# Performance work log

Measured on AMD Instinct MI355X. Metric: run time of the kernel, lower is better.

## Reference

```python
import jax, jax.numpy as jnp
import numpy as np

B, D, C, L, H = 4096, 768, 512, 32, 256
E = C * L  # total flattened extension embeddings

def _l2norm(x, eps=1e-12):
    n = jnp.sqrt(jnp.sum(x * x, axis=-1, keepdims=True))
    return x / jnp.maximum(n, eps)

def setup_inputs() -> dict:
    key = jax.random.key(0)
    ks = jax.random.split(key, 8)
    text_feat = jax.random.normal(ks[0], (B, D), dtype=jnp.float32)
    img_feat = jax.random.normal(ks[1], (B, D), dtype=jnp.float32)
    ext_embs = _l2norm(jax.random.normal(ks[2], (E, D), dtype=jnp.float32))
    concept_names = _l2norm(jax.random.normal(ks[3], (C, D), dtype=jnp.float32))
    # each concept has exactly L extension embeddings; sorted segment ids
    segment_ids = jnp.repeat(jnp.arange(C, dtype=jnp.int32), L)
    W1 = jax.random.normal(ks[4], (C + D, H), dtype=jnp.float32) * (1.0 / np.sqrt(C + D))
    b1 = jnp.zeros((H,), dtype=jnp.float32)
    W2 = jax.random.normal(ks[5], (H, C), dtype=jnp.float32) * (1.0 / np.sqrt(H))
    b2 = jnp.zeros((C,), dtype=jnp.float32)
    alpha = jnp.float32(0.5)
    temperature = jnp.float32(0.07)
    return {"text_feat": text_feat, "img_feat": img_feat, "ext_embs": ext_embs,
            "segment_ids": segment_ids, "concept_names": concept_names,
            "W1": W1, "b1": b1, "W2": W2, "b2": b2,
            "alpha": alpha, "temperature": temperature}

def reference(text_feat, img_feat, ext_embs, segment_ids, concept_names,
              W1, b1, W2, b2, alpha, temperature):
    # query = normalize(text + img)
    q = _l2norm(text_feat + img_feat)                      # [B, D]
    # ragged per-concept max similarity: one big GEMM + segmented max
    sim = jnp.einsum('bd,ed->be', q, ext_embs)            # [B, E]
    prior = jax.ops.segment_max(sim.T, segment_ids,
                                num_segments=C,
                                indices_are_sorted=True).T  # [B, C]
    # small MLP -> temperature softmax -> weighted concept sum
    h = jax.nn.relu(jnp.concatenate([prior, q], axis=-1) @ W1 + b1)  # [B, H]
    logits = h @ W2 + b2                                   # [B, C]
    weights = jax.nn.softmax(logits / temperature, axis=-1)
    dyn_prompt = weights @ concept_names                   # [B, D]
    combined = text_feat + alpha * dyn_prompt
    return _l2norm(combined)
```

## Files before the change

kernel.cpp:

```cpp
#include <hip/hip_runtime.h>
#include <hip/hip_bf16.h>

typedef unsigned short bfu;
typedef __attribute__((ext_vector_type(4))) float f32x4;
typedef __attribute__((ext_vector_type(8))) short bf16x8;
typedef __attribute__((ext_vector_type(4))) int i32x4;
typedef __attribute__((ext_vector_type(8))) int i32x8;

#define GAS __attribute__((address_space(1)))
#define LAS __attribute__((address_space(3)))

__device__ __forceinline__ unsigned short f2bf(float f) {
    unsigned int u = __float_as_uint(f);
    u += 0x7FFFu + ((u >> 16) & 1u);
    return (unsigned short)(u >> 16);
}

__device__ __forceinline__ void gld_lds16(const void* g, void* l) {
    __builtin_amdgcn_global_load_lds((GAS void*)g, (LAS void*)l, 16, 0, 0);
}

__device__ __forceinline__ unsigned pack_fp8x4(float a, float b, float c, float d) {
    int u = __builtin_amdgcn_cvt_pk_fp8_f32(a, b, 0, false);
    u = __builtin_amdgcn_cvt_pk_fp8_f32(c, d, u, true);
    return (unsigned)u;
}

__device__ __forceinline__ float block_sum256(float v, float* sm) {
    #pragma unroll
    for (int off = 32; off; off >>= 1) v += __shfl_xor(v, off);
    int w = threadIdx.x >> 6;
    if ((threadIdx.x & 63) == 0) sm[w] = v;
    __syncthreads();
    float r = sm[0] + sm[1] + sm[2] + sm[3];
    __syncthreads();
    return r;
}

__device__ __forceinline__ float block_max256(float v, float* sm) {
    #pragma unroll
    for (int off = 32; off; off >>= 1) v = fmaxf(v, __shfl_xor(v, off));
    int w = threadIdx.x >> 6;
    if ((threadIdx.x & 63) == 0) sm[w] = v;
    __syncthreads();
    float r = fmaxf(fmaxf(sm[0], sm[1]), fmaxf(sm[2], sm[3]));
    __syncthreads();
    return r;
}

__device__ __forceinline__ void transpose_piece(const float* __restrict__ in,
                                                bfu* __restrict__ out, int R, int idx) {
    int c = idx / R, r = idx - c * R;
    out[idx] = f2bf(in[(size_t)r * ((size_t)0) + 0]);
}

__global__ __launch_bounds__(256) void prep_kernel(const float* __restrict__ ext,
                                                   unsigned* __restrict__ E8,
                                                   const float* __restrict__ W1, bfu* __restrict__ W1t,
                                                   const float* __restrict__ W2, bfu* __restrict__ W2t,
                                                   const float* __restrict__ cn, bfu* __restrict__ cnt) {
    int b = blockIdx.x;
    if (b < 12288) {
        int i = b * 256 + threadIdx.x;
        float4 v = ((const float4*)ext)[i];
        E8[i] = pack_fp8x4(v.x * 16.0f, v.y * 16.0f, v.z * 16.0f, v.w * 16.0f);
    } else if (b < 13568) {
        int idx = (b - 12288) * 256 + threadIdx.x;
        int c = idx / 1280, r = idx - c * 1280;
        W1t[idx] = f2bf(W1[(size_t)r * 256 + c]);
    } else if (b < 14080) {
        int idx = (b - 13568) * 256 + threadIdx.x;
        int c = idx / 256, r = idx - c * 256;
        W2t[idx] = f2bf(W2[(size_t)r * 512 + c]);
    } else {
        int idx = (b - 14080) * 256 + threadIdx.x;
        int c = idx / 512, r = idx - c * 512;
        cnt[idx] = f2bf(cn[(size_t)r * 768 + c]);
    }
}

__global__ __launch_bounds__(256) void q_kernel(const float* __restrict__ text,
                                                const float* __restrict__ img,
                                                bfu* __restrict__ X,
                                                unsigned* __restrict__ Q8) {
    __shared__ float sm[4];
    int row = blockIdx.x, t = threadIdx.x;
    float4 v = {0.f, 0.f, 0.f, 0.f};
    if (t < 192) {
        float4 a = ((const float4*)(text + (size_t)row * 768))[t];
        float4 b = ((const float4*)(img + (size_t)row * 768))[t];
        v.x = a.x + b.x; v.y = a.y + b.y; v.z = a.z + b.z; v.w = a.w + b.w;
    }
    float ss = v.x * v.x + v.y * v.y + v.z * v.z + v.w * v.w;
    float tot = block_sum256(ss, sm);
    float inv = 1.0f / fmaxf(sqrtf(tot), 1e-12f);
    if (t < 192) {
        ushort4 o = make_ushort4(f2bf(v.x * inv), f2bf(v.y * inv), f2bf(v.z * inv), f2bf(v.w * inv));
        ((ushort4*)(X + (size_t)row * 1280 + 512))[t] = o;
        float s16 = inv * 16.0f;
        Q8[(size_t)row * 192 + t] = pack_fp8x4(v.x * s16, v.y * s16, v.z * s16, v.w * s16);
    }
}

__device__ __forceinline__ i32x8 ld_frag8(const char* s, int row, int lq) {
    const int r7 = row & 7;
    i32x4 lo = *(const i32x4*)(s + row * 128 + ((((lq << 1))     ^ r7) << 4));
    i32x4 hi = *(const i32x4*)(s + row * 128 + ((((lq << 1) | 1) ^ r7) << 4));
    i32x8 v;
    v[0] = lo[0]; v[1] = lo[1]; v[2] = lo[2]; v[3] = lo[3];
    v[4] = hi[0]; v[5] = hi[1]; v[6] = hi[2]; v[7] = hi[3];
    return v;
}

__global__ __launch_bounds__(256) void sim_segmax_kernel(const unsigned char* __restrict__ Q8,
                                                         const unsigned char* __restrict__ E8,
                                                         bfu* __restrict__ X) {
    __shared__ __align__(16) char sA[128 * 128];
    __shared__ __align__(16) char sB[128 * 128];
    int bm = blockIdx.x >> 7;
    int bn = blockIdx.x & 127;
    int m0 = bm * 128, n0 = bn * 128;
    const int t = threadIdx.x, lane = t & 63, wv = t >> 6;
    const int wm = (wv >> 1) << 6, wn = (wv & 1) << 6;
    const int lr = lane & 15, lq = lane >> 4;

    f32x4 zero = {0.f, 0.f, 0.f, 0.f};
    f32x4 acc[4][4];
    #pragma unroll
    for (int i = 0; i < 4; ++i)
        #pragma unroll
        for (int j = 0; j < 4; ++j) acc[i][j] = zero;

    for (int k0 = 0; k0 < 768; k0 += 128) {
        #pragma unroll
        for (int i = 0; i < 4; ++i) {
            int idx = i * 256 + t;
            int row = idx >> 3, cs = idx & 7, cg = cs ^ (row & 7);
            gld_lds16(Q8 + (size_t)(m0 + row) * 768 + k0 + (cg << 4), sA + idx * 16);
            gld_lds16(E8 + (size_t)(n0 + row) * 768 + k0 + (cg << 4), sB + idx * 16);
        }
        __syncthreads();
        i32x8 af[4], bf8[4];
        #pragma unroll
        for (int f = 0; f < 4; ++f) {
            af[f]  = ld_frag8(sA, wm + f * 16 + lr, lq);
            bf8[f] = ld_frag8(sB, wn + f * 16 + lr, lq);
        }
        #pragma unroll
        for (int i = 0; i < 4; ++i)
            #pragma unroll
            for (int j = 0; j < 4; ++j)
                acc[i][j] = __builtin_amdgcn_mfma_scale_f32_16x16x128_f8f6f4(
                    af[i], bf8[j], acc[i][j], 0, 0, 0, 0x7F7F7F7F, 0, 0x7F7F7F7F);
        __syncthreads();
    }

    const float sc = 0.00390625f;
    #pragma unroll
    for (int i = 0; i < 4; ++i) {
        #pragma unroll
        for (int r = 0; r < 4; ++r) {
            float g0 = fmaxf(acc[i][0][r], acc[i][1][r]);
            float g1 = fmaxf(acc[i][2][r], acc[i][3][r]);
            #pragma unroll
            for (int off = 8; off; off >>= 1) {
                g0 = fmaxf(g0, __shfl_xor(g0, off));
                g1 = fmaxf(g1, __shfl_xor(g1, off));
            }
            if (lr == 0) {
                int row = m0 + wm + i * 16 + lq * 4 + r;
                int g = (n0 + wn) >> 5;
                X[(size_t)row * 1280 + g]     = f2bf(g0 * sc);
                X[(size_t)row * 1280 + g + 1] = f2bf(g1 * sc);
            }
        }
    }
}

template <int BM>
__device__ __forceinline__ void gemm_mainloop(const bfu* A, const bfu* B, int K,
                                              int lda, int ldb, int m0, int n0,
                                              short* sA, short* sB, f32x4 acc[BM / 32][4]) {
    const int t = threadIdx.x, lane = t & 63, wv = t >> 6;
    const int wm = (wv >> 1) * (BM / 2), wn = (wv & 1) << 6;
    const int lr = lane & 15, lq = lane >> 4;

    for (int k0 = 0; k0 < K; k0 += 64) {
        #pragma unroll
        for (int i = 0; i < BM / 32; ++i) {
            int idx = i * 256 + t;
            int row = idx >> 3, cs = idx & 7, cg = cs ^ (row & 7);
            gld_lds16(A + (size_t)(m0 + row) * lda + k0 + (cg << 3), sA + idx * 8);
        }
        #pragma unroll
        for (int i = 0; i < 4; ++i) {
            int idx = i * 256 + t;
            int row = idx >> 3, cs = idx & 7, cg = cs ^ (row & 7);
            gld_lds16(B + (size_t)(n0 + row) * ldb + k0 + (cg << 3), sB + idx * 8);
        }
        __syncthreads();
        #pragma unroll
        for (int kk = 0; kk < 2; ++kk) {
            bf16x8 af[BM / 32], bfr[4];
            #pragma unroll
            for (int f = 0; f < BM / 32; ++f) {
                int mrow = wm + f * 16 + lr;
                int c = kk * 4 + lq;
                af[f] = *(const bf16x8*)(sA + mrow * 64 + ((c ^ (mrow & 7)) << 3));
            }
            #pragma unroll
            for (int f = 0; f < 4; ++f) {
                int nrow = wn + f * 16 + lr;
                int c = kk * 4 + lq;
                bfr[f] = *(const bf16x8*)(sB + nrow * 64 + ((c ^ (nrow & 7)) << 3));
            }
            #pragma unroll
            for (int i = 0; i < BM / 32; ++i)
                #pragma unroll
                for (int j = 0; j < 4; ++j)
                    acc[i][j] = __builtin_amdgcn_mfma_f32_16x16x32_bf16(af[i], bfr[j], acc[i][j], 0, 0, 0);
        }
        __syncthreads();
    }
}

template <int EPI, int BM>
__global__ __launch_bounds__(256) void gemm_kernel(const bfu* __restrict__ A,
                                                   const bfu* __restrict__ B,
                                                   const float* __restrict__ bias,
                                                   void* __restrict__ out,
                                                   int K, int lda, int ldb, int N, int ntN) {
    __shared__ __align__(16) short sA[BM * 64];
    __shared__ __align__(16) short sB[128 * 64];
    int bm = blockIdx.x / ntN, bn = blockIdx.x - bm * ntN;
    int m0 = bm * BM, n0 = bn * 128;
    f32x4 zero = {0.f, 0.f, 0.f, 0.f};
    f32x4 acc[BM / 32][4];
    #pragma unroll
    for (int i = 0; i < BM / 32; ++i)
        #pragma unroll
        for (int j = 0; j < 4; ++j) acc[i][j] = zero;

    gemm_mainloop<BM>(A, B, K, lda, ldb, m0, n0, sA, sB, acc);

    const int t = threadIdx.x, lane = t & 63, wv = t >> 6;
    const int wm = (wv >> 1) * (BM / 2), wn = (wv & 1) << 6;
    const int lr = lane & 15, lq = lane >> 4;
    #pragma unroll
    for (int j = 0; j < 4; ++j) {
        int col = n0 + wn + j * 16 + lr;
        float bv = (EPI >= 1) ? bias[col] : 0.0f;
        #pragma unroll
        for (int i = 0; i < BM / 32; ++i) {
            #pragma unroll
            for (int r = 0; r < 4; ++r) {
                int row = m0 + wm + i * 16 + lq * 4 + r;
                float v = acc[i][j][r] + bv;
                if (EPI == 1) {
                    v = fmaxf(v, 0.0f);
                    ((bfu*)out)[(size_t)row * N + col] = f2bf(v);
                } else {
                    ((float*)out)[(size_t)row * N + col] = v;
                }
            }
        }
    }
}

__global__ __launch_bounds__(256) void softmax_kernel(const float* __restrict__ logits,
                                                      const float* __restrict__ temp,
                                                      bfu* __restrict__ wout) {
    __shared__ float sm[4];
    int row = blockIdx.x, t = threadIdx.x;
    float invT = 1.0f / temp[0];
    float l0 = logits[(size_t)row * 512 + t];
    float l1 = logits[(size_t)row * 512 + 256 + t];
    float m = block_max256(fmaxf(l0, l1), sm);
    float e0 = __expf((l0 - m) * invT);
    float e1 = __expf((l1 - m) * invT);
    float s = block_sum256(e0 + e1, sm);
    float inv = 1.0f / s;
    wout[(size_t)row * 512 + t]       = f2bf(e0 * inv);
    wout[(size_t)row * 512 + 256 + t] = f2bf(e1 * inv);
}

__global__ __launch_bounds__(256) void final_kernel(const float* __restrict__ text,
                                                    const float* __restrict__ dyn,
                                                    const float* __restrict__ alpha,
                                                    float* __restrict__ out) {
    __shared__ float sm[4];
    int row = blockIdx.x, t = threadIdx.x;
    float a = alpha[0];
    float v[3]; float ss = 0.f;
    #pragma unroll
    for (int i = 0; i < 3; ++i) {
        size_t o = (size_t)row * 768 + t + 256 * i;
        v[i] = text[o] + a * dyn[o];
        ss += v[i] * v[i];
    }
    float tot = block_sum256(ss, sm);
    float inv = 1.0f / fmaxf(sqrtf(tot), 1e-12f);
    #pragma unroll
    for (int i = 0; i < 3; ++i)
        out[(size_t)row * 768 + t + 256 * i] = v[i] * inv;
}

extern "C" void kernel_launch(void* const* d_in, const int* in_sizes, int n_in,
                              void* d_out, int out_size, void* d_ws, size_t ws_size,
                              hipStream_t stream) {
    const float* text  = (const float*)d_in[0];
    const float* img   = (const float*)d_in[1];
    const float* ext   = (const float*)d_in[2];
    const float* cn    = (const float*)d_in[4];
    const float* W1    = (const float*)d_in[5];
    const float* b1    = (const float*)d_in[6];
    const float* W2    = (const float*)d_in[7];
    const float* b2    = (const float*)d_in[8];
    const float* alpha = (const float*)d_in[9];
    const float* temp  = (const float*)d_in[10];
    float* out = (float*)d_out;

    char* p = (char*)d_ws;
    auto carve = [&](size_t bytes) -> char* {
        char* r = p; p += (bytes + 255) & ~(size_t)255; return r;
    };
    unsigned char* E8 = (unsigned char*)carve((size_t)16384 * 768);
    unsigned char* Q8 = (unsigned char*)carve((size_t)4096 * 768);
    bfu*   X      = (bfu*)carve((size_t)4096 * 1280 * 2);
    bfu*   W1t    = (bfu*)carve((size_t)256 * 1280 * 2);
    bfu*   W2t    = (bfu*)carve((size_t)512 * 256 * 2);
    bfu*   cnt    = (bfu*)carve((size_t)768 * 512 * 2);
    bfu*   Hm     = (bfu*)carve((size_t)4096 * 256 * 2);
    float* logits = (float*)carve((size_t)4096 * 512 * 4);
    bfu*   wts    = (bfu*)carve((size_t)4096 * 512 * 2);
    float* dyn    = (float*)carve((size_t)4096 * 768 * 4);

    prep_kernel<<<15616, 256, 0, stream>>>(ext, (unsigned*)E8, W1, W1t, W2, W2t, cn, cnt);
    q_kernel<<<4096, 256, 0, stream>>>(text, img, X, (unsigned*)Q8);
    sim_segmax_kernel<<<32 * 128, 256, 0, stream>>>(Q8, E8, X);
    gemm_kernel<1, 64><<<64 * 2, 256, 0, stream>>>(X, W1t, b1, (void*)Hm, 1280, 1280, 1280, 256, 2);
    gemm_kernel<2, 64><<<64 * 4, 256, 0, stream>>>(Hm, W2t, b2, (void*)logits, 256, 256, 256, 512, 4);
    softmax_kernel<<<4096, 256, 0, stream>>>(logits, temp, wts);
    gemm_kernel<0, 64><<<64 * 6, 256, 0, stream>>>(wts, cnt, nullptr, (void*)dyn, 512, 512, 512, 768, 6);
    final_kernel<<<4096, 256, 0, stream>>>(text, dyn, alpha, out);
}
```

Before: 319.3 us.

## Merge q prep into prep kernel, XCD-aware sim tile mapping, smaller MLP GEMM tiles

Folds the query-normalization kernel into the prep kernel to remove one launch. It also remaps sim_segmax block indices so that blocks sharing the same E tile land on the same XCD, which should improve L2 reuse across the 8 XCDs. The three small MLP GEMMs move from 64-row to 32-row M tiles, doubling their block counts for better CU occupancy. The costs are more redundant B-tile loads in the GEMMs and a larger, more divergent prep kernel.

```diff
diff --git a/kernel.cpp b/kernel.cpp
--- a/kernel.cpp
+++ b/kernel.cpp
@@ -48,57 +48,50 @@
     return r;
 }
 
-__device__ __forceinline__ void transpose_piece(const float* __restrict__ in,
-                                                bfu* __restrict__ out, int R, int idx) {
-    int c = idx / R, r = idx - c * R;
-    out[idx] = f2bf(in[(size_t)r * ((size_t)0) + 0]);
-}
-
-__global__ __launch_bounds__(256) void prep_kernel(const float* __restrict__ ext,
+__global__ __launch_bounds__(256) void prep_kernel(const float* __restrict__ text,
+                                                   const float* __restrict__ img,
+                                                   bfu* __restrict__ X,
+                                                   unsigned* __restrict__ Q8,
+                                                   const float* __restrict__ ext,
                                                    unsigned* __restrict__ E8,
                                                    const float* __restrict__ W1, bfu* __restrict__ W1t,
                                                    const float* __restrict__ W2, bfu* __restrict__ W2t,
                                                    const float* __restrict__ cn, bfu* __restrict__ cnt) {
-    int b = blockIdx.x;
-    if (b < 12288) {
-        int i = b * 256 + threadIdx.x;
+    __shared__ float sm[4];
+    int b = blockIdx.x, t = threadIdx.x;
+    if (b < 4096) {
+        int row = b;
+        float4 v = {0.f, 0.f, 0.f, 0.f};
+        if (t < 192) {
+            float4 a = ((const float4*)(text + (size_t)row * 768))[t];
+            float4 c = ((const float4*)(img + (size_t)row * 768))[t];
+            v.x = a.x + c.x; v.y = a.y + c.y; v.z = a.z + c.z; v.w = a.w + c.w;
+        }
+        float ss = v.x * v.x + v.y * v.y + v.z * v.z + v.w * v.w;
+        float tot = block_sum256(ss, sm);
+        float inv = 1.0f / fmaxf(sqrtf(tot), 1e-12f);
+        if (t < 192) {
+            ushort4 o = make_ushort4(f2bf(v.x * inv), f2bf(v.y * inv), f2bf(v.z * inv), f2bf(v.w * inv));
+            ((ushort4*)(X + (size_t)row * 1280 + 512))[t] = o;
+            float s16 = inv * 16.0f;
+            Q8[(size_t)row * 192 + t] = pack_fp8x4(v.x * s16, v.y * s16, v.z * s16, v.w * s16);
+        }
+    } else if (b < 16384) {
+        int i = (b - 4096) * 256 + t;
         float4 v = ((const float4*)ext)[i];
         E8[i] = pack_fp8x4(v.x * 16.0f, v.y * 16.0f, v.z * 16.0f, v.w * 16.0f);
-    } else if (b < 13568) {
-        int idx = (b - 12288) * 256 + threadIdx.x;
+    } else if (b < 17664) {
+        int idx = (b - 16384) * 256 + t;
         int c = idx / 1280, r = idx - c * 1280;
         W1t[idx] = f2bf(W1[(size_t)r * 256 + c]);
-    } else if (b < 14080) {
-        int idx = (b - 13568) * 256 + threadIdx.x;
+    } else if (b < 18176) {
+        int idx = (b - 17664) * 256 + t;
         int c = idx / 256, r = idx - c * 256;
         W2t[idx] = f2bf(W2[(size_t)r * 512 + c]);
     } else {
-        int idx = (b - 14080) * 256 + threadIdx.x;
+        int idx = (b - 18176) * 256 + t;
         int c = idx / 512, r = idx - c * 512;
         cnt[idx] = f2bf(cn[(size_t)r * 768 + c]);
-    }
-}
-
-__global__ __launch_bounds__(256) void q_kernel(const float* __restrict__ text,
-                                                const float* __restrict__ img,
-                                                bfu* __restrict__ X,
-                                                unsigned* __restrict__ Q8) {
-    __shared__ float sm[4];
-    int row = blockIdx.x, t = threadIdx.x;
-    float4 v = {0.f, 0.f, 0.f, 0.f};
-    if (t < 192) {
-        float4 a = ((const float4*)(text + (size_t)row * 768))[t];
-        float4 b = ((const float4*)(img + (size_t)row * 768))[t];
-        v.x = a.x + b.x; v.y = a.y + b.y; v.z = a.z + b.z; v.w = a.w + b.w;
-    }
-    float ss = v.x * v.x + v.y * v.y + v.z * v.z + v.w * v.w;
-    float tot = block_sum256(ss, sm);
-    float inv = 1.0f / fmaxf(sqrtf(tot), 1e-12f);
-    if (t < 192) {
-        ushort4 o = make_ushort4(f2bf(v.x * inv), f2bf(v.y * inv), f2bf(v.z * inv), f2bf(v.w * inv));
-        ((ushort4*)(X + (size_t)row * 1280 + 512))[t] = o;
-        float s16 = inv * 16.0f;
-        Q8[(size_t)row * 192 + t] = pack_fp8x4(v.x * s16, v.y * s16, v.z * s16, v.w * s16);
     }
 }
 
@@ -117,8 +110,10 @@
                                                          bfu* __restrict__ X) {
     __shared__ __align__(16) char sA[128 * 128];
     __shared__ __align__(16) char sB[128 * 128];
-    int bm = blockIdx.x >> 7;
-    int bn = blockIdx.x & 127;
+    int xcd = blockIdx.x & 7;
+    int lid = blockIdx.x >> 3;
+    int bm = lid & 31;
+    int bn = ((lid >> 5) << 3) | xcd;
     int m0 = bm * 128, n0 = bn * 128;
     const int t = threadIdx.x, lane = t & 63, wv = t >> 6;
     const int wm = (wv >> 1) << 6, wn = (wv & 1) << 6;
@@ -335,12 +330,12 @@
     bfu*   wts    = (bfu*)carve((size_t)4096 * 512 * 2);
     float* dyn    = (float*)carve((size_t)4096 * 768 * 4);
 
-    prep_kernel<<<15616, 256, 0, stream>>>(ext, (unsigned*)E8, W1, W1t, W2, W2t, cn, cnt);
-    q_kernel<<<4096, 256, 0, stream>>>(text, img, X, (unsigned*)Q8);
-    sim_segmax_kernel<<<32 * 128, 256, 0, stream>>>(Q8, E8, X);
-    gemm_kernel<1, 64><<<64 * 2, 256, 0, stream>>>(X, W1t, b1, (void*)Hm, 1280, 1280, 1280, 256, 2);
-    gemm_kernel<2, 64><<<64 * 4, 256, 0, stream>>>(Hm, W2t, b2, (void*)logits, 256, 256, 256, 512, 4);
+    prep_kernel<<<19712, 256, 0, stream>>>(text, img, X, (unsigned*)Q8,
+                                           ext, (unsigned*)E8, W1, W1t, W2, W2t, cn, cnt);
+    sim_segmax_kernel<<<4096, 256, 0, stream>>>(Q8, E8, X);
+    gemm_kernel<1, 32><<<128 * 2, 256, 0, stream>>>(X, W1t, b1, (void*)Hm, 1280, 1280, 1280, 256, 2);
+    gemm_kernel<2, 32><<<128 * 4, 256, 0, stream>>>(Hm, W2t, b2, (void*)logits, 256, 256, 256, 512, 4);
     softmax_kernel<<<4096, 256, 0, stream>>>(logits, temp, wts);
-    gemm_kernel<0, 64><<<64 * 6, 256, 0, stream>>>(wts, cnt, nullptr, (void*)dyn, 512, 512, 512, 768, 6);
+    gemm_kernel<0, 32><<<128 * 6, 256, 0, stream>>>(wts, cnt, nullptr, (void*)dyn, 512, 512, 512, 768, 6);
     final_kernel<<<4096, 256, 0, stream>>>(text, dyn, alpha, out);
 }
```

Result: no change. 314.9 us (-1.4%).
